# Kernel tuning notes

Hardware: AMD Instinct MI355X
Metric: run time of the kernel (lower is better)

The kernel has to match this reference:

```python
import jax, jax.numpy as jnp
import numpy as np

D_MODEL = 1024
HEADS = 16
D_K = D_MODEL // HEADS
MAX_LEN = 2048
SCALE = 1.0 / np.sqrt(D_K)


def setup_inputs() -> dict:
    key = jax.random.key(0)
    ks = jax.random.split(key, 12)
    S, B = 2048, 2
    lin = lambda k: jax.random.normal(k, (D_MODEL, D_MODEL), jnp.float32) * (1.0 / np.sqrt(D_MODEL))
    return {
        "query": jax.random.normal(ks[0], (S, B, D_MODEL), jnp.float32),
        "key": jax.random.normal(ks[1], (S, B, D_MODEL), jnp.float32),
        "value": jax.random.normal(ks[2], (S, B, D_MODEL), jnp.float32),
        "Wq": lin(ks[3]), "bq": jnp.zeros((D_MODEL,), jnp.float32),
        "Wk": lin(ks[4]), "bk": jnp.zeros((D_MODEL,), jnp.float32),
        "Wv": lin(ks[5]), "bv": jnp.zeros((D_MODEL,), jnp.float32),
        "Wo": lin(ks[6]), "bo": jnp.zeros((D_MODEL,), jnp.float32),
        "rel_table": jax.random.normal(ks[7], (2 * MAX_LEN - 1, HEADS), jnp.float32),
    }


def reference(query, key, value, Wq, bq, Wk, bk, Wv, bv, Wo, bo, rel_table):
    q_len, B, _ = query.shape
    k_len = key.shape[0]
    # projections (torch Linear: x @ W.T + b)
    q = (query @ Wq.T + bq).reshape(q_len, B, HEADS, D_K)
    k = (key @ Wk.T + bk).reshape(k_len, B, HEADS, D_K)
    v = (value @ Wv.T + bv).reshape(k_len, B, HEADS, D_K)
    scores = jnp.einsum('qbhd,kbhd->bhqk', q, k) * SCALE
    # relative position bias gather
    dist = jnp.arange(q_len)[:, None] - jnp.arange(k_len)[None, :] + (MAX_LEN - 1)
    dist = jnp.clip(dist, 0, 2 * MAX_LEN - 2)
    bias = rel_table[dist]                     # [q,k,h]
    scores = scores + jnp.transpose(bias, (2, 0, 1))[None]  # [1,h,q,k]
    attn = jax.nn.softmax(scores, axis=-1)
    out = jnp.einsum('bhqk,kbhd->qbhd', attn, v).reshape(q_len, B, D_MODEL)
    return out @ Wo.T + bo
```

## Files before the change

kernel.cpp:

```cpp
#include <hip/hip_runtime.h>
#include <hip/hip_bf16.h>

typedef __bf16 bf16_t;
typedef __bf16 bf16x8 __attribute__((ext_vector_type(8)));
typedef __bf16 bf16x4 __attribute__((ext_vector_type(4)));
typedef float f32x4 __attribute__((ext_vector_type(4)));

#define D_MODEL 1024
#define HEADS 16
#define D_K 64
#define SEQ 2048
#define BATCH 2
#define MTOT (SEQ * BATCH)
#define LOG2E 1.4426950408889634f
#define QSCALE (0.125f * LOG2E)

#define GLDS16(g, l)                                                        \
  __builtin_amdgcn_global_load_lds(                                        \
      (const __attribute__((address_space(1))) unsigned int*)(g),          \
      (__attribute__((address_space(3))) unsigned int*)(l), 16, 0, 0)

__global__ __launch_bounds__(256) void cvt_all(const float* q, const float* k,
                                               const float* v, const float* wq,
                                               const float* wk, const float* wv,
                                               const float* wo, bf16_t* xq, bf16_t* xk,
                                               bf16_t* xv, bf16_t* wqkv, bf16_t* wob) {
  const size_t nIn = (size_t)MTOT * D_MODEL;
  const size_t nW = (size_t)D_MODEL * D_MODEL;
  size_t e = ((size_t)blockIdx.x * 256 + threadIdx.x) * 8;
  const float* s;
  bf16_t* d;
  size_t off;
  if (e < 3 * nIn) {
    int j = (int)(e >> 22);
    off = e & (nIn - 1);
    s = j == 0 ? q : (j == 1 ? k : v);
    d = j == 0 ? xq : (j == 1 ? xk : xv);
  } else {
    size_t e2 = e - 3 * nIn;
    int j = (int)(e2 >> 20);
    off = e2 & (nW - 1);
    s = j == 0 ? wq : (j == 1 ? wk : (j == 2 ? wv : wo));
    d = j == 3 ? wob : (wqkv + (size_t)j * nW);
  }
  float4 a = *(const float4*)(s + off);
  float4 b = *(const float4*)(s + off + 4);
  bf16x8 o;
  o[0] = (bf16_t)a.x; o[1] = (bf16_t)a.y; o[2] = (bf16_t)a.z; o[3] = (bf16_t)a.w;
  o[4] = (bf16_t)b.x; o[5] = (bf16_t)b.y; o[6] = (bf16_t)b.z; o[7] = (bf16_t)b.w;
  *(bf16x8*)(d + off) = o;
}

__global__ __launch_bounds__(512, 2) void gemm_qkv(const bf16_t* __restrict__ Xq,
                                                   const bf16_t* __restrict__ Xk,
                                                   const bf16_t* __restrict__ Xv,
                                                   const bf16_t* __restrict__ Wqkv,
                                                   const float* __restrict__ bq,
                                                   const float* __restrict__ bk,
                                                   const float* __restrict__ bv,
                                                   bf16_t* __restrict__ qa,
                                                   bf16_t* __restrict__ ka,
                                                   bf16_t* __restrict__ vt) {
  __shared__ __align__(16) bf16_t As[3][128 * 64];
  __shared__ __align__(16) bf16_t Bs[3][128 * 64];
  const int t = threadIdx.x;
  const int f = blockIdx.x;
  const int xcd = f & 7, fi = f >> 3;
  const int by = xcd * 4 + (fi & 3);
  const int col = fi >> 2;
  const int seg = col >> 3;
  const bf16_t* X = seg == 0 ? Xq : (seg == 1 ? Xk : Xv);
  const float* bias = seg == 0 ? bq : (seg == 1 ? bk : bv);
  const float scale = seg == 0 ? QSCALE : 1.0f;
  const int m0 = by * 128;
  const int n0g = col * 128;
  const int w = t >> 6, l = t & 63, lr = l & 15, lg = l >> 4;
  const int wm = (w >> 2) * 64, wn = (w & 3) * 32;

  f32x4 acc[4][2] = {};

  const int srow0 = t >> 3;
  const int sck = (((t & 7) ^ (srow0 & 7)) << 3);
  const int sx = (lr & 7) << 4;

#define QKV_STAGE(buf, kt)                                                      \
  {                                                                             \
    _Pragma("unroll") for (int p = 0; p < 2; ++p) {                             \
      int row = (p * 512 + t) >> 3;                                             \
      int wb = (p * 512 + w * 64) * 8;                                          \
      GLDS16(&X[(size_t)(m0 + row) * D_MODEL + (kt) + sck], As[buf] + wb);      \
      GLDS16(&Wqkv[(size_t)(n0g + row) * D_MODEL + (kt) + sck], Bs[buf] + wb);  \
    }                                                                           \
  }

  QKV_STAGE(0, 0);
  QKV_STAGE(1, 64);

  int cur = 0;
  for (int step = 0; step < 16; ++step) {
    if (step < 15)
      asm volatile("s_waitcnt vmcnt(4)" ::: "memory");
    else
      asm volatile("s_waitcnt vmcnt(0)" ::: "memory");
    __builtin_amdgcn_s_barrier();
    if (step + 2 < 16) {
      int nb = cur + 2; nb = nb >= 3 ? nb - 3 : nb;
      QKV_STAGE(nb, (step + 2) * 64);
    }
#pragma unroll
    for (int kk = 0; kk < 2; ++kk) {
      bf16x8 a[4], b[2];
#pragma unroll
      for (int i = 0; i < 4; ++i)
        a[i] = *(const bf16x8*)((const char*)As[cur] + (wm + i * 16 + lr) * 128 +
                                ((kk * 64 + lg * 16) ^ sx));
#pragma unroll
      for (int j = 0; j < 2; ++j)
        b[j] = *(const bf16x8*)((const char*)Bs[cur] + (wn + j * 16 + lr) * 128 +
                                ((kk * 64 + lg * 16) ^ sx));
      __builtin_amdgcn_s_setprio(1);
#pragma unroll
      for (int i = 0; i < 4; ++i)
#pragma unroll
        for (int j = 0; j < 2; ++j)
          acc[i][j] = __builtin_amdgcn_mfma_f32_16x16x32_bf16(a[i], b[j], acc[i][j], 0, 0, 0);
      __builtin_amdgcn_s_setprio(0);
    }
    cur = cur + 1 >= 3 ? 0 : cur + 1;
  }
#undef QKV_STAGE

#pragma unroll
  for (int i = 0; i < 4; ++i) {
#pragma unroll
    for (int j = 0; j < 2; ++j) {
      int lc = ((n0g + wn) & 1023) + j * 16 + lr;
      float bb = bias[lc];
      int h = lc >> 6, d = lc & 63;
#pragma unroll
      for (int ii = 0; ii < 4; ++ii) {
        int row = m0 + wm + i * 16 + lg * 4 + ii;
        float v = (acc[i][j][ii] + bb) * scale;
        int s = row >> 1, b2 = row & 1;
        if (seg == 2)
          vt[(((size_t)(b2 * HEADS + h) * D_K) + d) * SEQ + s] = (bf16_t)v;
        else if (seg == 1)
          ka[(((size_t)(b2 * HEADS + h) * SEQ) + s) * D_K + d] = (bf16_t)v;
        else
          qa[(((size_t)(b2 * HEADS + h) * SEQ) + s) * D_K + d] = (bf16_t)v;
      }
    }
  }
}

__global__ __launch_bounds__(512) void gemm_out(const bf16_t* __restrict__ X,
                                                const bf16_t* __restrict__ W,
                                                const float* __restrict__ bias,
                                                float* __restrict__ out) {
  __shared__ __align__(16) bf16_t As[2][128 * 64];
  __shared__ __align__(16) bf16_t Bs[2][128 * 64];
  const int t = threadIdx.x;
  const int f = blockIdx.x;
  const int xcd = f & 7, fi = f >> 3;
  const int by = xcd * 4 + (fi & 3);
  const int bx = fi >> 2;
  const int m0 = by * 128, n0 = bx * 128;
  const int w = t >> 6, l = t & 63, lr = l & 15, lg = l >> 4;
  const int wm = (w >> 2) * 64, wn = (w & 3) * 32;
  const int srow0 = t >> 3;
  const int sck = (((t & 7) ^ (srow0 & 7)) << 3);
  const int sx = (lr & 7) << 4;

  f32x4 acc[4][2] = {};

#define OUT_STAGE(buf, kt)                                                      \
  {                                                                             \
    _Pragma("unroll") for (int p = 0; p < 2; ++p) {                             \
      int row = (p * 512 + t) >> 3;                                             \
      int wb = (p * 512 + w * 64) * 8;                                          \
      GLDS16(&X[(size_t)(m0 + row) * D_MODEL + (kt) + sck], As[buf] + wb);      \
      GLDS16(&W[(size_t)(n0 + row) * D_MODEL + (kt) + sck], Bs[buf] + wb);      \
    }                                                                           \
  }

  OUT_STAGE(0, 0);
  __syncthreads();

  for (int step = 0; step < 16; ++step) {
    const int cur = step & 1;
    if (step + 1 < 16) OUT_STAGE(cur ^ 1, (step + 1) * 64);
#pragma unroll
    for (int kk = 0; kk < 2; ++kk) {
      bf16x8 a[4], b[2];
#pragma unroll
      for (int i = 0; i < 4; ++i)
        a[i] = *(const bf16x8*)((const char*)As[cur] + (wm + i * 16 + lr) * 128 +
                                ((kk * 64 + lg * 16) ^ sx));
#pragma unroll
      for (int j = 0; j < 2; ++j)
        b[j] = *(const bf16x8*)((const char*)Bs[cur] + (wn + j * 16 + lr) * 128 +
                                ((kk * 64 + lg * 16) ^ sx));
#pragma unroll
      for (int i = 0; i < 4; ++i)
#pragma unroll
        for (int j = 0; j < 2; ++j)
          acc[i][j] = __builtin_amdgcn_mfma_f32_16x16x32_bf16(a[i], b[j], acc[i][j], 0, 0, 0);
    }
    __syncthreads();
  }
#undef OUT_STAGE

#pragma unroll
  for (int i = 0; i < 4; ++i) {
#pragma unroll
    for (int j = 0; j < 2; ++j) {
      int col = n0 + wn + j * 16 + lr;
      float bb = bias[col];
#pragma unroll
      for (int ii = 0; ii < 4; ++ii) {
        int row = m0 + wm + i * 16 + lg * 4 + ii;
        out[(size_t)row * D_MODEL + col] = acc[i][j][ii] + bb;
      }
    }
  }
}

#define QBLK 128
#define KVBLK 64
#define NT (SEQ / KVBLK)
#define TBL_N 2175
#define LDP 72

__global__ __launch_bounds__(512, 4) void attn_kernel(const bf16_t* __restrict__ Qa,
                                                      const bf16_t* __restrict__ Ka,
                                                      const bf16_t* __restrict__ Vt,
                                                      const float* __restrict__ rel,
                                                      bf16_t* __restrict__ ctx) {
  __shared__ float rbl[TBL_N + 1];
  __shared__ __align__(16) bf16_t ks[2][KVBLK * 64];
  __shared__ __align__(16) bf16_t vs[2][KVBLK * 64];
  __shared__ __align__(16) bf16_t p_lds[8][16 * LDP];

  const int f = blockIdx.x;
  const int nf = (f & 7) * 64 + (f >> 3);
  const int qb = nf & 15, bh = nf >> 4;
  const int h = bh & (HEADS - 1), b2 = bh >> 4;
  const int qbase = qb * QBLK;
  const int t = threadIdx.x, w = t >> 6, l = t & 63, lr = l & 15, lg = l >> 4;

  const bf16_t* Qbh = Qa + (size_t)bh * SEQ * D_K;
  const bf16_t* Kbh = Ka + (size_t)bh * SEQ * D_K;
  const bf16_t* Vbh = Vt + (size_t)bh * D_K * SEQ;

  for (int j = t; j < TBL_N; j += 512)
    rbl[j] = LOG2E * rel[(size_t)(qbase + (TBL_N - 1) - j) * HEADS + h];

  const int srow = t >> 3;
  const int scol = (((t & 7) ^ (srow & 7)) << 3);
  const int sldsoff = w * 512;

  const int qloc = w * 16 + lr;
  bf16x8 qf[2];
#pragma unroll
  for (int kk = 0; kk < 2; ++kk)
    qf[kk] = *(const bf16x8*)(&Qbh[(size_t)(qbase + qloc) * D_K + kk * 32 + lg * 8]);

  bf16x8 ones;
#pragma unroll
  for (int e = 0; e < 8; ++e) ones[e] = (bf16_t)1.0f;

  GLDS16(Kbh + (size_t)srow * D_K + scol, ks[0] + sldsoff);
  GLDS16(Vbh + (size_t)srow * SEQ + scol, vs[0] + sldsoff);
  __syncthreads();

  f32x4 acc_o[4] = {};
  f32x4 l_acc = {};
  bf16_t* pw = p_lds[w];
  const int sw = (lr & 7) << 4;
  const int roff = 127 - qloc + lg * 4;

  for (int it = 0; it < NT; ++it) {
    const int cur = it & 1;
    const int kt = it * KVBLK;
    if (it + 1 < NT) {
      const int ktn = kt + KVBLK;
      GLDS16(Kbh + (size_t)(ktn + srow) * D_K + scol, ks[cur ^ 1] + sldsoff);
      GLDS16(Vbh + (size_t)srow * SEQ + ktn + scol, vs[cur ^ 1] + sldsoff);
    }
    const char* Kc = (const char*)ks[cur];
    const char* Vc = (const char*)vs[cur];

#pragma unroll
    for (int c = 0; c < 4; ++c) {
      const int r0 = roff + kt + c * 16;
      f32x4 z;
      z[0] = rbl[r0]; z[1] = rbl[r0 + 1]; z[2] = rbl[r0 + 2]; z[3] = rbl[r0 + 3];
#pragma unroll
      for (int kk = 0; kk < 2; ++kk) {
        bf16x8 kf = *(const bf16x8*)(Kc + (c * 16 + lr) * 128 + ((kk * 64 + lg * 16) ^ sw));
        z = __builtin_amdgcn_mfma_f32_16x16x32_bf16(kf, qf[kk], z, 0, 0, 0);
      }
      bf16x4 pv;
#pragma unroll
      for (int i = 0; i < 4; ++i) pv[i] = (bf16_t)__builtin_amdgcn_exp2f(z[i]);
      *(bf16x4*)(&pw[lr * LDP + c * 16 + lg * 4]) = pv;
    }

    __builtin_amdgcn_s_setprio(1);
#pragma unroll
    for (int kk = 0; kk < 2; ++kk) {
      bf16x8 pa = *(const bf16x8*)(&pw[lr * LDP + kk * 32 + lg * 8]);
      l_acc = __builtin_amdgcn_mfma_f32_16x16x32_bf16(ones, pa, l_acc, 0, 0, 0);
#pragma unroll
      for (int c = 0; c < 4; ++c) {
        bf16x8 vf = *(const bf16x8*)(Vc + (c * 16 + lr) * 128 + ((kk * 64 + lg * 16) ^ sw));
        acc_o[c] = __builtin_amdgcn_mfma_f32_16x16x32_bf16(vf, pa, acc_o[c], 0, 0, 0);
      }
    }
    __builtin_amdgcn_s_setprio(0);
    __syncthreads();
  }

  const float inv = 1.0f / l_acc[0];

  int qg = qbase + qloc;
  size_t base = ((size_t)qg * BATCH + b2) * D_MODEL + h * D_K;
#pragma unroll
  for (int c = 0; c < 4; ++c) {
    bf16x4 ov;
#pragma unroll
    for (int ii = 0; ii < 4; ++ii) ov[ii] = (bf16_t)(acc_o[c][ii] * inv);
    *(bf16x4*)(&ctx[base + c * 16 + lg * 4]) = ov;
  }
}

extern "C" void kernel_launch(void* const* d_in, const int* in_sizes, int n_in,
                              void* d_out, int out_size, void* d_ws, size_t ws_size,
                              hipStream_t stream) {
  const float* query = (const float*)d_in[0];
  const float* key_i = (const float*)d_in[1];
  const float* value = (const float*)d_in[2];
  const float* Wq = (const float*)d_in[3];
  const float* bq = (const float*)d_in[4];
  const float* Wk = (const float*)d_in[5];
  const float* bk = (const float*)d_in[6];
  const float* Wv = (const float*)d_in[7];
  const float* bv = (const float*)d_in[8];
  const float* Wo = (const float*)d_in[9];
  const float* bo = (const float*)d_in[10];
  const float* rel = (const float*)d_in[11];
  float* out = (float*)d_out;

  char* ws = (char*)d_ws;
  size_t off = 0;
  auto alloc = [&](size_t bytes) {
    char* p = ws + off;
    off = (off + bytes + 255) & ~(size_t)255;
    return p;
  };
  const size_t nIn = (size_t)MTOT * D_MODEL;
  const size_t nW = (size_t)D_MODEL * D_MODEL;

  bf16_t* Xq = (bf16_t*)alloc(nIn * 2);
  bf16_t* Xk = (bf16_t*)alloc(nIn * 2);
  bf16_t* Xv = (bf16_t*)alloc(nIn * 2);
  bf16_t* Wqkv = (bf16_t*)alloc(3 * nW * 2);
  bf16_t* Wob = (bf16_t*)alloc(nW * 2);
  bf16_t* qa = (bf16_t*)alloc(nIn * 2);
  bf16_t* ka = (bf16_t*)alloc(nIn * 2);
  bf16_t* vt = (bf16_t*)alloc(nIn * 2);
  bf16_t* ctx = (bf16_t*)alloc(nIn * 2);

  cvt_all<<<dim3(8192), 256, 0, stream>>>(query, key_i, value, Wq, Wk, Wv, Wo, Xq, Xk,
                                          Xv, Wqkv, Wob);

  gemm_qkv<<<dim3(768), 512, 0, stream>>>(Xq, Xk, Xv, Wqkv, bq, bk, bv, qa, ka, vt);

  attn_kernel<<<dim3(512), 512, 0, stream>>>(qa, ka, vt, rel, ctx);

  gemm_out<<<dim3(256), 512, 0, stream>>>(ctx, Wob, bo, out);
}
```

Baseline: 130.9 us.

## Give each attention wave two 16-row query tiles to reuse K/V fragments

Measured after the change: 132.6 us. About the same (+1.4%).

```diff
diff --git a/kernel.cpp b/kernel.cpp
--- a/kernel.cpp
+++ b/kernel.cpp
@@ -231,7 +231,7 @@
 #define TBL_N 2175
 #define LDP 72
 
-__global__ __launch_bounds__(512, 4) void attn_kernel(const bf16_t* __restrict__ Qa,
+__global__ __launch_bounds__(256, 2) void attn_kernel(const bf16_t* __restrict__ Qa,
                                                       const bf16_t* __restrict__ Ka,
                                                       const bf16_t* __restrict__ Vt,
                                                       const float* __restrict__ rel,
@@ -239,7 +239,7 @@
   __shared__ float rbl[TBL_N + 1];
   __shared__ __align__(16) bf16_t ks[2][KVBLK * 64];
   __shared__ __align__(16) bf16_t vs[2][KVBLK * 64];
-  __shared__ __align__(16) bf16_t p_lds[8][16 * LDP];
+  __shared__ __align__(16) bf16_t p_lds[4][32 * LDP];
 
   const int f = blockIdx.x;
   const int nf = (f & 7) * 64 + (f >> 3);
@@ -252,40 +252,49 @@
   const bf16_t* Kbh = Ka + (size_t)bh * SEQ * D_K;
   const bf16_t* Vbh = Vt + (size_t)bh * D_K * SEQ;
 
-  for (int j = t; j < TBL_N; j += 512)
+  for (int j = t; j < TBL_N; j += 256)
     rbl[j] = LOG2E * rel[(size_t)(qbase + (TBL_N - 1) - j) * HEADS + h];
 
   const int srow = t >> 3;
   const int scol = (((t & 7) ^ (srow & 7)) << 3);
-  const int sldsoff = w * 512;
-
-  const int qloc = w * 16 + lr;
-  bf16x8 qf[2];
-#pragma unroll
-  for (int kk = 0; kk < 2; ++kk)
-    qf[kk] = *(const bf16x8*)(&Qbh[(size_t)(qbase + qloc) * D_K + kk * 32 + lg * 8]);
+
+  const int q0 = w * 32 + lr;
+  bf16x8 qf[2][2];
+#pragma unroll
+  for (int kk = 0; kk < 2; ++kk) {
+    qf[0][kk] = *(const bf16x8*)(&Qbh[(size_t)(qbase + q0) * D_K + kk * 32 + lg * 8]);
+    qf[1][kk] = *(const bf16x8*)(&Qbh[(size_t)(qbase + q0 + 16) * D_K + kk * 32 + lg * 8]);
+  }
 
   bf16x8 ones;
 #pragma unroll
   for (int e = 0; e < 8; ++e) ones[e] = (bf16_t)1.0f;
 
-  GLDS16(Kbh + (size_t)srow * D_K + scol, ks[0] + sldsoff);
-  GLDS16(Vbh + (size_t)srow * SEQ + scol, vs[0] + sldsoff);
+#pragma unroll
+  for (int p = 0; p < 2; ++p) {
+    GLDS16(Kbh + (size_t)(p * 32 + srow) * D_K + scol, ks[0] + p * 2048 + w * 512);
+    GLDS16(Vbh + (size_t)(p * 32 + srow) * SEQ + scol, vs[0] + p * 2048 + w * 512);
+  }
   __syncthreads();
 
-  f32x4 acc_o[4] = {};
-  f32x4 l_acc = {};
+  f32x4 acc_o[2][4] = {};
+  f32x4 l_acc[2] = {};
   bf16_t* pw = p_lds[w];
   const int sw = (lr & 7) << 4;
-  const int roff = 127 - qloc + lg * 4;
+  const int roff = 127 - q0 + lg * 4;
 
   for (int it = 0; it < NT; ++it) {
     const int cur = it & 1;
     const int kt = it * KVBLK;
     if (it + 1 < NT) {
       const int ktn = kt + KVBLK;
-      GLDS16(Kbh + (size_t)(ktn + srow) * D_K + scol, ks[cur ^ 1] + sldsoff);
-      GLDS16(Vbh + (size_t)srow * SEQ + ktn + scol, vs[cur ^ 1] + sldsoff);
+#pragma unroll
+      for (int p = 0; p < 2; ++p) {
+        GLDS16(Kbh + (size_t)(ktn + p * 32 + srow) * D_K + scol,
+               ks[cur ^ 1] + p * 2048 + w * 512);
+        GLDS16(Vbh + (size_t)(p * 32 + srow) * SEQ + ktn + scol,
+               vs[cur ^ 1] + p * 2048 + w * 512);
+      }
     }
     const char* Kc = (const char*)ks[cur];
     const char* Vc = (const char*)vs[cur];
@@ -293,44 +302,55 @@
 #pragma unroll
     for (int c = 0; c < 4; ++c) {
       const int r0 = roff + kt + c * 16;
-      f32x4 z;
-      z[0] = rbl[r0]; z[1] = rbl[r0 + 1]; z[2] = rbl[r0 + 2]; z[3] = rbl[r0 + 3];
+      f32x4 z0, z1;
+      z0[0] = rbl[r0];      z0[1] = rbl[r0 + 1];  z0[2] = rbl[r0 + 2];  z0[3] = rbl[r0 + 3];
+      z1[0] = rbl[r0 - 16]; z1[1] = rbl[r0 - 15]; z1[2] = rbl[r0 - 14]; z1[3] = rbl[r0 - 13];
 #pragma unroll
       for (int kk = 0; kk < 2; ++kk) {
         bf16x8 kf = *(const bf16x8*)(Kc + (c * 16 + lr) * 128 + ((kk * 64 + lg * 16) ^ sw));
-        z = __builtin_amdgcn_mfma_f32_16x16x32_bf16(kf, qf[kk], z, 0, 0, 0);
-      }
-      bf16x4 pv;
-#pragma unroll
-      for (int i = 0; i < 4; ++i) pv[i] = (bf16_t)__builtin_amdgcn_exp2f(z[i]);
-      *(bf16x4*)(&pw[lr * LDP + c * 16 + lg * 4]) = pv;
+        z0 = __builtin_amdgcn_mfma_f32_16x16x32_bf16(kf, qf[0][kk], z0, 0, 0, 0);
+        z1 = __builtin_amdgcn_mfma_f32_16x16x32_bf16(kf, qf[1][kk], z1, 0, 0, 0);
+      }
+      bf16x4 pv0, pv1;
+#pragma unroll
+      for (int i = 0; i < 4; ++i) {
+        pv0[i] = (bf16_t)__builtin_amdgcn_exp2f(z0[i]);
+        pv1[i] = (bf16_t)__builtin_amdgcn_exp2f(z1[i]);
+      }
+      *(bf16x4*)(&pw[lr * LDP + c * 16 + lg * 4]) = pv0;
+      *(bf16x4*)(&pw[(16 + lr) * LDP + c * 16 + lg * 4]) = pv1;
     }
 
     __builtin_amdgcn_s_setprio(1);
 #pragma unroll
     for (int kk = 0; kk < 2; ++kk) {
-      bf16x8 pa = *(const bf16x8*)(&pw[lr * LDP + kk * 32 + lg * 8]);
-      l_acc = __builtin_amdgcn_mfma_f32_16x16x32_bf16(ones, pa, l_acc, 0, 0, 0);
+      bf16x8 pa0 = *(const bf16x8*)(&pw[lr * LDP + kk * 32 + lg * 8]);
+      bf16x8 pa1 = *(const bf16x8*)(&pw[(16 + lr) * LDP + kk * 32 + lg * 8]);
+      l_acc[0] = __builtin_amdgcn_mfma_f32_16x16x32_bf16(ones, pa0, l_acc[0], 0, 0, 0);
+      l_acc[1] = __builtin_amdgcn_mfma_f32_16x16x32_bf16(ones, pa1, l_acc[1], 0, 0, 0);
 #pragma unroll
       for (int c = 0; c < 4; ++c) {
         bf16x8 vf = *(const bf16x8*)(Vc + (c * 16 + lr) * 128 + ((kk * 64 + lg * 16) ^ sw));
-        acc_o[c] = __builtin_amdgcn_mfma_f32_16x16x32_bf16(vf, pa, acc_o[c], 0, 0, 0);
+        acc_o[0][c] = __builtin_amdgcn_mfma_f32_16x16x32_bf16(vf, pa0, acc_o[0][c], 0, 0, 0);
+        acc_o[1][c] = __builtin_amdgcn_mfma_f32_16x16x32_bf16(vf, pa1, acc_o[1][c], 0, 0, 0);
       }
     }
     __builtin_amdgcn_s_setprio(0);
     __syncthreads();
   }
 
-  const float inv = 1.0f / l_acc[0];
-
-  int qg = qbase + qloc;
-  size_t base = ((size_t)qg * BATCH + b2) * D_MODEL + h * D_K;
-#pragma unroll
-  for (int c = 0; c < 4; ++c) {
-    bf16x4 ov;
-#pragma unroll
-    for (int ii = 0; ii < 4; ++ii) ov[ii] = (bf16_t)(acc_o[c][ii] * inv);
-    *(bf16x4*)(&ctx[base + c * 16 + lg * 4]) = ov;
+#pragma unroll
+  for (int s = 0; s < 2; ++s) {
+    const float inv = 1.0f / l_acc[s][0];
+    int qg = qbase + q0 + s * 16;
+    size_t base = ((size_t)qg * BATCH + b2) * D_MODEL + h * D_K;
+#pragma unroll
+    for (int c = 0; c < 4; ++c) {
+      bf16x4 ov;
+#pragma unroll
+      for (int ii = 0; ii < 4; ++ii) ov[ii] = (bf16_t)(acc_o[s][c][ii] * inv);
+      *(bf16x4*)(&ctx[base + c * 16 + lg * 4]) = ov;
+    }
   }
 }
 
@@ -376,7 +396,7 @@
 
   gemm_qkv<<<dim3(768), 512, 0, stream>>>(Xq, Xk, Xv, Wqkv, bq, bk, bv, qa, ka, vt);
 
-  attn_kernel<<<dim3(512), 512, 0, stream>>>(qa, ka, vt, rel, ctx);
+  attn_kernel<<<dim3(512), 256, 0, stream>>>(qa, ka, vt, rel, ctx);
 
   gemm_out<<<dim3(256), 512, 0, stream>>>(ctx, Wob, bo, out);
 }
```
